# Optimization experiments

Measured on AMD Instinct MI355X. Metric: run time of the kernel, lower is better.

The kernel has to match this reference:

```python
import jax, jax.numpy as jnp
import numpy as np

NEG_INF = -1.0e9  # matches the -1000000000.0 additive mask in the source


def setup_inputs() -> dict:
    key = jax.random.key(0)
    kq, kk, kv = jax.random.split(key, 3)
    B, Lq, Lk, D = 16, 2048, 2048, 128
    q = jax.random.normal(kq, (B, Lq, D), dtype=jnp.float32)
    k = jax.random.normal(kk, (B, Lk, D), dtype=jnp.float32)
    v = jax.random.normal(kv, (B, Lk, D), dtype=jnp.float32)
    mask = jnp.ones((B, Lq, Lk), dtype=jnp.int32)  # 1 = attend, 0 = blocked
    return {"q": q, "k": k, "v": v, "mask": mask}


def reference(q, k, v, mask):
    # temper = sqrt(d_k)
    temper = jnp.sqrt(jnp.asarray(q.shape[-1], dtype=jnp.float32))
    # scores: [B, Lq, Lk] = batch_dot(q, k, axes=[2,2]) / temper
    scores = jnp.einsum("bqd,bkd->bqk", q, k) / temper
    # additive mask: -1e9 * (1 - mask)
    scores = scores + NEG_INF * (1.0 - mask.astype(jnp.float32))
    attn = jax.nn.softmax(scores, axis=-1)
    # dropout is identity at inference time
    out = jnp.einsum("bqk,bkd->bqd", attn, v)
    return (out, attn)
```

## Files before the change

kernel.cpp:

```cpp
#include <hip/hip_runtime.h>

typedef __bf16 bf16_t;
typedef __bf16 bf16x8 __attribute__((ext_vector_type(8)));
typedef __bf16 bf16x4 __attribute__((ext_vector_type(4)));
typedef float  f32x4  __attribute__((ext_vector_type(4)));
typedef int    i32x4  __attribute__((ext_vector_type(4)));

#define B_      16
#define L_      2048
#define D_      128
#define QTB     128
#define NEGINF  (-1.0e9f)
#define SCALE   0.08838834764831845f

#define MFMA_BF16 __builtin_amdgcn_mfma_f32_16x16x32_bf16

#define BARRIER() do { asm volatile("s_waitcnt lgkmcnt(0)" ::: "memory"); \
                       __builtin_amdgcn_s_barrier(); } while (0)

__global__ __launch_bounds__(256) void prep_kernel(
    const float* __restrict__ k, const float* __restrict__ v,
    bf16_t* __restrict__ kb, bf16_t* __restrict__ vt)
{
    __shared__ bf16_t tile[128 * 144];
    const int tid = threadIdx.x;
    const int bid = (int)blockIdx.x;

    if (bid < 256) {
        const int b  = bid >> 4;
        const int l0 = (bid & 15) * 128;
        #pragma unroll
        for (int it = 0; it < 16; ++it) {
            int idx = tid + it * 256;
            int row = idx >> 5;
            int dc4 = idx & 31;
            f32x4 x = __builtin_nontemporal_load(
                (const f32x4*)(v + ((size_t)b * L_ + l0 + row) * (size_t)D_ + dc4 * 4));
            #pragma unroll
            for (int i = 0; i < 4; ++i) tile[(dc4 * 4 + i) * 144 + row] = (bf16_t)x[i];
        }
        __syncthreads();
        #pragma unroll
        for (int it = 0; it < 8; ++it) {
            int idx = tid + it * 256;
            int d   = idx >> 4;
            int lc  = idx & 15;
            bf16x8 vec = *(const bf16x8*)&tile[d * 144 + lc * 8];
            *(bf16x8*)(vt + ((size_t)b * D_ + d) * (size_t)L_ + l0 + lc * 8) = vec;
        }
    } else {
        const int idx0 = (bid - 256) * 256 + tid;
        #pragma unroll
        for (int c = 0; c < 16; ++c) {
            int idx = idx0 + c * 65536;
            f32x4 x = __builtin_nontemporal_load((const f32x4*)(k + (size_t)idx * 4));
            bf16x4 o;
            #pragma unroll
            for (int i = 0; i < 4; ++i) o[i] = (bf16_t)x[i];
            *(bf16x4*)(kb + (size_t)idx * 4) = o;
        }
    }
}

template <bool WS>
__global__ __launch_bounds__(512, 1) void sdpa_kernel(
    const float* __restrict__ q, const float* __restrict__ k,
    const float* __restrict__ v, const int* __restrict__ mask,
    const bf16_t* __restrict__ kb, const bf16_t* __restrict__ vt,
    float* __restrict__ out, float* __restrict__ attn)
{
    __shared__ char     KstRaw[3 * 8192];
    __shared__ char     MVRaw[3 * 16384];
    __shared__ unsigned mlds[8 * 1024];
    __shared__ bf16_t   plds[8][16][40];

    const int tid = threadIdx.x;
    const int w   = tid >> 6;
    const int l   = tid & 63;
    const int li  = l & 15;
    const int lg  = l >> 4;

    const int bid  = (int)blockIdx.x;
    const int bid2 = (bid & 7) * 32 + (bid >> 3);
    const int b    = bid2 >> 4;
    const int qt   = bid2 & 15;
    const int qbase = qt * QTB;

    const size_t bq   = (size_t)b * L_;
    const int    qrow = qbase + w * 16 + li;

    const float*  qp   = q  + (bq + qbase) * (size_t)D_;
    const bf16_t* kbp  = kb + bq * (size_t)D_;
    const float*  kp   = k  + bq * (size_t)D_;
    const bf16_t* vtp  = vt + (size_t)b * D_ * (size_t)L_;
    const float*  vp   = v  + bq * (size_t)D_;
    float* attnrow = attn + (bq + qrow) * (size_t)L_;
    float* outp    = out  + (bq + qbase) * (size_t)D_;

    bf16x8 aq[4];
    #pragma unroll
    for (int ds = 0; ds < 4; ++ds) {
        const float* p = qp + (size_t)(w * 16 + li) * D_ + ds * 32 + lg * 8;
        f32x4 x0 = *(const f32x4*)p;
        f32x4 x1 = *(const f32x4*)(p + 4);
        bf16x8 a;
        #pragma unroll
        for (int u = 0; u < 4; ++u) {
            a[u]     = (bf16_t)(x0[u] * SCALE);
            a[4 + u] = (bf16_t)(x1[u] * SCALE);
        }
        aq[ds] = a;
    }

    const int krow = tid >> 4, kslot = tid & 15;
    const int kdst = krow * 256 + ((kslot * 16) ^ ((krow & 7) << 4));
    const int mrow = tid >> 3, mslot = tid & 7;
    const int mdst0 = mrow * 128 + ((mslot * 16) ^ ((mrow & 7) << 4));
    const int mdst1 = (mrow + 64) * 128 + ((mslot * 16) ^ ((mrow & 7) << 4));
    const int vrow = tid >> 2, vslot = tid & 3;
    const int vdst = vrow * 64 + vslot * 16;

    const bf16_t* ksrcb = kbp + (size_t)krow * D_ + kslot * 8;
    const float*  ksrcf = kp  + (size_t)krow * D_ + kslot * 8;
    const int*    msrc0 = mask + (size_t)(bq + qbase + mrow) * L_ + mslot * 4;
    const int*    msrc1 = mask + (size_t)(bq + qbase + mrow + 64) * L_ + mslot * 4;
    const bf16_t* vsrcb = vtp + (size_t)vrow * L_ + vslot * 8;

    auto issueK = [&](int c, i32x4& ri, f32x4& rf0, f32x4& rf1) {
        if constexpr (WS) {
            ri = *(const i32x4*)(ksrcb + (size_t)c * 32 * D_);
        } else {
            rf0 = *(const f32x4*)(ksrcf + (size_t)c * 32 * D_);
            rf1 = *(const f32x4*)(ksrcf + (size_t)c * 32 * D_ + 4);
        }
    };
    auto writeK = [&](int sl, const i32x4& ri, const f32x4& rf0, const f32x4& rf1) {
        char* d = KstRaw + sl * 8192 + kdst;
        if constexpr (WS) {
            *(i32x4*)d = ri;
        } else {
            bf16x8 o;
            #pragma unroll
            for (int u = 0; u < 4; ++u) { o[u] = (bf16_t)rf0[u]; o[4+u] = (bf16_t)rf1[u]; }
            *(bf16x8*)d = o;
        }
    };
    auto issueM = [&](int c, i32x4& m0, i32x4& m1) {
        m0 = __builtin_nontemporal_load((const i32x4*)(msrc0 + c * 32));
        m1 = __builtin_nontemporal_load((const i32x4*)(msrc1 + c * 32));
    };
    auto writeM = [&](int sl, const i32x4& m0, const i32x4& m1) {
        *(i32x4*)(MVRaw + sl * 16384 + mdst0) = m0;
        *(i32x4*)(MVRaw + sl * 16384 + mdst1) = m1;
    };
    auto issueV = [&](int c, i32x4& ri, float (&vf)[8]) {
        if constexpr (WS) {
            ri = *(const i32x4*)(vsrcb + c * 32);
        } else {
            #pragma unroll
            for (int u = 0; u < 8; ++u)
                vf[u] = vp[(size_t)(c * 32 + vslot * 8 + u) * D_ + vrow];
        }
    };
    auto writeV = [&](int sl, const i32x4& ri, const float (&vf)[8]) {
        char* d = MVRaw + sl * 16384 + vdst;
        if constexpr (WS) {
            *(i32x4*)d = ri;
        } else {
            bf16x8 o;
            #pragma unroll
            for (int u = 0; u < 8; ++u) o[u] = (bf16_t)vf[u];
            *(bf16x8*)d = o;
        }
    };

    const int xr = (li & 7) << 4;

    auto qkt = [&](int sl, f32x4& a0, f32x4& a1) {
        const char* Ks = KstRaw + sl * 8192;
        f32x4 r0 = {0.f,0.f,0.f,0.f}, r1 = {0.f,0.f,0.f,0.f};
        #pragma unroll
        for (int ds = 0; ds < 4; ++ds) {
            bf16x8 k0 = *(const bf16x8*)(Ks + li * 256 + ((ds * 64 + lg * 16) ^ xr));
            r0 = MFMA_BF16(k0, aq[ds], r0, 0, 0, 0);
        }
        #pragma unroll
        for (int ds = 0; ds < 4; ++ds) {
            bf16x8 k1 = *(const bf16x8*)(Ks + (16 + li) * 256 + ((ds * 64 + lg * 16) ^ xr));
            r1 = MFMA_BF16(k1, aq[ds], r1, 0, 0, 0);
        }
        a0 = r0; a1 = r1;
    };

    float m_run = -3.4e38f, l_run = 0.f;
    {
        unsigned mword = 0;
        auto p1c = [&](int c, int sl) {
            f32x4 a0, a1;
            qkt(sl, a0, a1);
            const char* Ms = MVRaw + sl * 16384 + (w * 16 + li) * 128;
            i32x4 va  = *(const i32x4*)(Ms + ((lg * 16) ^ xr));
            i32x4 vb_ = *(const i32x4*)(Ms + ((64 + lg * 16) ^ xr));
            unsigned byte =
                (va[0]  != 0 ?   1u : 0u) | (va[1]  != 0 ?   2u : 0u) |
                (va[2]  != 0 ?   4u : 0u) | (va[3]  != 0 ?   8u : 0u) |
                (vb_[0] != 0 ?  16u : 0u) | (vb_[1] != 0 ?  32u : 0u) |
                (vb_[2] != 0 ?  64u : 0u) | (vb_[3] != 0 ? 128u : 0u);
            float s0[4], s1[4];
            #pragma unroll
            for (int r = 0; r < 4; ++r) {
                s0[r] = a0[r] + (((byte >> r)       & 1u) ? 0.f : NEGINF);
                s1[r] = a1[r] + (((byte >> (4 + r)) & 1u) ? 0.f : NEGINF);
            }
            float mx = fmaxf(fmaxf(fmaxf(s0[0], s0[1]), fmaxf(s0[2], s0[3])),
                             fmaxf(fmaxf(s1[0], s1[1]), fmaxf(s1[2], s1[3])));
            mx = fmaxf(mx, m_run);
            float acc = 0.f;
            #pragma unroll
            for (int r = 0; r < 4; ++r)
                acc += __expf(s0[r] - mx) + __expf(s1[r] - mx);
            l_run = l_run * __expf(m_run - mx) + acc;
            m_run = mx;
            mword |= byte << ((c & 3) * 8);
            if ((c & 3) == 3) { mlds[w * 1024 + (c >> 2) * 64 + l] = mword; mword = 0; }
        };

        i32x4 kA{}, kB{}, mA0{}, mA1{}, mB0{}, mB1{};
        f32x4 kfA0{}, kfA1{}, kfB0{}, kfB1{};
        issueK(0, kA, kfA0, kfA1); issueM(0, mA0, mA1);
        issueK(1, kB, kfB0, kfB1); issueM(1, mB0, mB1);
        writeK(0, kA, kfA0, kfA1); writeM(0, mA0, mA1);
        BARRIER();
        int s0i = 0, s1i = 1, s2i = 2;
        #pragma unroll 1
        for (int c = 0; c < 64; c += 2) {
            if (c + 2 < 64) { issueK(c + 2, kA, kfA0, kfA1); issueM(c + 2, mA0, mA1); }
            writeK(s1i, kB, kfB0, kfB1); writeM(s1i, mB0, mB1);
            BARRIER();
            p1c(c, s0i);
            { int t = s0i; s0i = s1i; s1i = s2i; s2i = t; }
            if (c + 3 < 64) { issueK(c + 3, kB, kfB0, kfB1); issueM(c + 3, mB0, mB1); }
            if (c + 2 < 64) { writeK(s1i, kA, kfA0, kfA1); writeM(s1i, mA0, mA1); }
            BARRIER();
            p1c(c + 1, s0i);
            { int t = s0i; s0i = s1i; s1i = s2i; s2i = t; }
        }
    }

    #pragma unroll
    for (int off = 16; off < 64; off <<= 1) {
        float mo = __shfl_xor(m_run, off);
        float lo = __shfl_xor(l_run, off);
        float mn = fmaxf(m_run, mo);
        l_run = l_run * __expf(m_run - mn) + lo * __expf(mo - mn);
        m_run = mn;
    }
    const float inv_l = 1.f / l_run;

    f32x4 pv[8];
    #pragma unroll
    for (int dt = 0; dt < 8; ++dt) pv[dt] = {0.f, 0.f, 0.f, 0.f};

    {
        auto p2c = [&](int c, int sl) {
            f32x4 a0, a1;
            qkt(sl, a0, a1);
            const unsigned mw = mlds[w * 1024 + (c >> 2) * 64 + l];
            const unsigned byte = (mw >> ((c & 3) * 8)) & 0xffu;
            f32x4 o0, o1; bf16x4 pb0, pb1;
            #pragma unroll
            for (int r = 0; r < 4; ++r) {
                float sa = a0[r] + (((byte >> r)       & 1u) ? 0.f : NEGINF);
                float sb = a1[r] + (((byte >> (4 + r)) & 1u) ? 0.f : NEGINF);
                float p0 = __expf(sa - m_run);
                float p1 = __expf(sb - m_run);
                o0[r] = p0 * inv_l;  o1[r] = p1 * inv_l;
                pb0[r] = (bf16_t)p0; pb1[r] = (bf16_t)p1;
            }
            __builtin_nontemporal_store(o0, (f32x4*)(attnrow + c * 32 + lg * 4));
            __builtin_nontemporal_store(o1, (f32x4*)(attnrow + c * 32 + 16 + lg * 4));
            *(bf16x4*)&plds[w][li][lg * 4]      = pb0;
            *(bf16x4*)&plds[w][li][16 + lg * 4] = pb1;
            bf16x8 pa = *(const bf16x8*)&plds[w][li][lg * 8];
            const char* Vs = MVRaw + sl * 16384;
            #pragma unroll
            for (int dt = 0; dt < 8; ++dt) {
                bf16x8 vbf = *(const bf16x8*)(Vs + (dt * 16 + li) * 64 + lg * 16);
                pv[dt] = MFMA_BF16(pa, vbf, pv[dt], 0, 0, 0);
            }
        };

        BARRIER();
        i32x4 kA{}, kB{}, vA{}, vB{};
        f32x4 kfA0{}, kfA1{}, kfB0{}, kfB1{};
        float vfA[8], vfB[8];
        issueK(0, kA, kfA0, kfA1); issueV(0, vA, vfA);
        issueK(1, kB, kfB0, kfB1); issueV(1, vB, vfB);
        writeK(0, kA, kfA0, kfA1); writeV(0, vA, vfA);
        BARRIER();
        int s0i = 0, s1i = 1, s2i = 2;
        #pragma unroll 1
        for (int c = 0; c < 64; c += 2) {
            if (c + 2 < 64) { issueK(c + 2, kA, kfA0, kfA1); issueV(c + 2, vA, vfA); }
            writeK(s1i, kB, kfB0, kfB1); writeV(s1i, vB, vfB);
            BARRIER();
            p2c(c, s0i);
            { int t = s0i; s0i = s1i; s1i = s2i; s2i = t; }
            if (c + 3 < 64) { issueK(c + 3, kB, kfB0, kfB1); issueV(c + 3, vB, vfB); }
            if (c + 2 < 64) { writeK(s1i, kA, kfA0, kfA1); writeV(s1i, vA, vfA); }
            BARRIER();
            p2c(c + 1, s0i);
            { int t = s0i; s0i = s1i; s1i = s2i; s2i = t; }
        }
    }

    #pragma unroll
    for (int r = 0; r < 4; ++r) {
        const float il = __shfl(inv_l, lg * 4 + r);
        float* orow = outp + (size_t)(w * 16 + lg * 4 + r) * D_ + li;
        #pragma unroll
        for (int dt = 0; dt < 8; ++dt)
            __builtin_nontemporal_store(pv[dt][r] * il, orow + dt * 16);
    }
}

extern "C" void kernel_launch(void* const* d_in, const int* in_sizes, int n_in,
                              void* d_out, int out_size, void* d_ws, size_t ws_size,
                              hipStream_t stream) {
    const float* q    = (const float*)d_in[0];
    const float* k    = (const float*)d_in[1];
    const float* v    = (const float*)d_in[2];
    const int*   mask = (const int*)d_in[3];

    float* out  = (float*)d_out;
    float* attn = out + (size_t)B_ * L_ * D_;

    const size_t VT_BYTES = (size_t)B_ * D_ * L_ * 2;
    const size_t KB_BYTES = (size_t)B_ * L_ * D_ * 2;
    const bool ws_ok = ws_size >= VT_BYTES + KB_BYTES;
    bf16_t* vt = (bf16_t*)d_ws;
    bf16_t* kb = (bf16_t*)((char*)d_ws + VT_BYTES);

    if (ws_ok) {
        hipLaunchKernelGGL(prep_kernel, dim3(512), dim3(256), 0, stream, k, v, kb, vt);
        hipLaunchKernelGGL(sdpa_kernel<true>, dim3(256), dim3(512), 0, stream,
                           q, k, v, mask, kb, vt, out, attn);
    } else {
        hipLaunchKernelGGL(sdpa_kernel<false>, dim3(256), dim3(512), 0, stream,
                           q, k, v, mask, kb, vt, out, attn);
    }
}
```

Baseline: 183.2 us.

## Halve query tile to 64 rows, launch 512 blocks of 256 threads

```diff
diff --git a/kernel.cpp b/kernel.cpp
--- a/kernel.cpp
+++ b/kernel.cpp
@@ -9,7 +9,7 @@
 #define B_      16
 #define L_      2048
 #define D_      128
-#define QTB     128
+#define QTB     64
 #define NEGINF  (-1.0e9f)
 #define SCALE   0.08838834764831845f
 
@@ -63,16 +63,16 @@
 }
 
 template <bool WS>
-__global__ __launch_bounds__(512, 1) void sdpa_kernel(
+__global__ __launch_bounds__(256, 1) void sdpa_kernel(
     const float* __restrict__ q, const float* __restrict__ k,
     const float* __restrict__ v, const int* __restrict__ mask,
     const bf16_t* __restrict__ kb, const bf16_t* __restrict__ vt,
     float* __restrict__ out, float* __restrict__ attn)
 {
-    __shared__ char     KstRaw[3 * 8192];
-    __shared__ char     MVRaw[3 * 16384];
-    __shared__ unsigned mlds[8 * 1024];
-    __shared__ bf16_t   plds[8][16][40];
+    __shared__ char     Kst[3][8192];
+    __shared__ char     Vst[3][8192];
+    __shared__ unsigned mbits[64 * 64];
+    __shared__ bf16_t   plds[4][16][40];
 
     const int tid = threadIdx.x;
     const int w   = tid >> 6;
@@ -81,20 +81,19 @@
     const int lg  = l >> 4;
 
     const int bid  = (int)blockIdx.x;
-    const int bid2 = (bid & 7) * 32 + (bid >> 3);
-    const int b    = bid2 >> 4;
-    const int qt   = bid2 & 15;
+    const int bid2 = (bid & 7) * 64 + (bid >> 3);
+    const int b    = bid2 >> 5;
+    const int qt   = bid2 & 31;
     const int qbase = qt * QTB;
 
-    const size_t bq   = (size_t)b * L_;
-    const int    qrow = qbase + w * 16 + li;
+    const size_t bq = (size_t)b * L_;
 
     const float*  qp   = q  + (bq + qbase) * (size_t)D_;
     const bf16_t* kbp  = kb + bq * (size_t)D_;
     const float*  kp   = k  + bq * (size_t)D_;
     const bf16_t* vtp  = vt + (size_t)b * D_ * (size_t)L_;
     const float*  vp   = v  + bq * (size_t)D_;
-    float* attnrow = attn + (bq + qrow) * (size_t)L_;
+    float* attnrow = attn + (bq + qbase + (size_t)(w * 16 + li)) * (size_t)L_;
     float* outp    = out  + (bq + qbase) * (size_t)D_;
 
     bf16x8 aq[4];
@@ -112,72 +111,87 @@
         aq[ds] = a;
     }
 
-    const int krow = tid >> 4, kslot = tid & 15;
-    const int kdst = krow * 256 + ((kslot * 16) ^ ((krow & 7) << 4));
-    const int mrow = tid >> 3, mslot = tid & 7;
-    const int mdst0 = mrow * 128 + ((mslot * 16) ^ ((mrow & 7) << 4));
-    const int mdst1 = (mrow + 64) * 128 + ((mslot * 16) ^ ((mrow & 7) << 4));
-    const int vrow = tid >> 2, vslot = tid & 3;
-    const int vdst = vrow * 64 + vslot * 16;
-
-    const bf16_t* ksrcb = kbp + (size_t)krow * D_ + kslot * 8;
-    const float*  ksrcf = kp  + (size_t)krow * D_ + kslot * 8;
-    const int*    msrc0 = mask + (size_t)(bq + qbase + mrow) * L_ + mslot * 4;
-    const int*    msrc1 = mask + (size_t)(bq + qbase + mrow + 64) * L_ + mslot * 4;
-    const bf16_t* vsrcb = vtp + (size_t)vrow * L_ + vslot * 8;
-
-    auto issueK = [&](int c, i32x4& ri, f32x4& rf0, f32x4& rf1) {
+    const int krow = tid >> 3, ks = tid & 7;
+    const int kdst = krow * 256 + ((ks * 16) ^ ((krow & 7) << 4));
+    const bf16_t* ksrcb = kbp + (size_t)krow * D_ + ks * 8;
+    const float*  ksrcf = kp  + (size_t)krow * D_ + ks * 8;
+
+    const int vrow = tid >> 1, vs = tid & 1;
+    const int vswz = (vrow >> 1) & 3;
+    const int vdst0 = vrow * 64 + (((vs * 2)     ^ vswz) << 4);
+    const int vdst1 = vrow * 64 + (((vs * 2 + 1) ^ vswz) << 4);
+    const bf16_t* vsrcb = vtp + (size_t)vrow * L_;
+
+    const int mr = tid & 63;
+    const int* msrc = mask + (size_t)(bq + qbase + mr) * L_ + w * 8;
+
+    auto issueK = [&](int c, i32x4& r0, i32x4& r1, f32x4* rf) {
         if constexpr (WS) {
-            ri = *(const i32x4*)(ksrcb + (size_t)c * 32 * D_);
+            r0 = *(const i32x4*)(ksrcb + (size_t)c * 32 * D_);
+            r1 = *(const i32x4*)(ksrcb + (size_t)c * 32 * D_ + 64);
         } else {
-            rf0 = *(const f32x4*)(ksrcf + (size_t)c * 32 * D_);
-            rf1 = *(const f32x4*)(ksrcf + (size_t)c * 32 * D_ + 4);
-        }
-    };
-    auto writeK = [&](int sl, const i32x4& ri, const f32x4& rf0, const f32x4& rf1) {
-        char* d = KstRaw + sl * 8192 + kdst;
+            rf[0] = *(const f32x4*)(ksrcf + (size_t)c * 32 * D_);
+            rf[1] = *(const f32x4*)(ksrcf + (size_t)c * 32 * D_ + 4);
+            rf[2] = *(const f32x4*)(ksrcf + (size_t)c * 32 * D_ + 64);
+            rf[3] = *(const f32x4*)(ksrcf + (size_t)c * 32 * D_ + 68);
+        }
+    };
+    auto writeK = [&](int sl, const i32x4& r0, const i32x4& r1, const f32x4* rf) {
+        char* d = Kst[sl] + kdst;
         if constexpr (WS) {
-            *(i32x4*)d = ri;
+            *(i32x4*)d = r0;
+            *(i32x4*)(d + 128) = r1;
         } else {
-            bf16x8 o;
-            #pragma unroll
-            for (int u = 0; u < 4; ++u) { o[u] = (bf16_t)rf0[u]; o[4+u] = (bf16_t)rf1[u]; }
-            *(bf16x8*)d = o;
+            bf16x8 o0, o1;
+            #pragma unroll
+            for (int u = 0; u < 4; ++u) {
+                o0[u] = (bf16_t)rf[0][u]; o0[4+u] = (bf16_t)rf[1][u];
+                o1[u] = (bf16_t)rf[2][u]; o1[4+u] = (bf16_t)rf[3][u];
+            }
+            *(bf16x8*)d = o0;
+            *(bf16x8*)(d + 128) = o1;
         }
     };
     auto issueM = [&](int c, i32x4& m0, i32x4& m1) {
-        m0 = __builtin_nontemporal_load((const i32x4*)(msrc0 + c * 32));
-        m1 = __builtin_nontemporal_load((const i32x4*)(msrc1 + c * 32));
-    };
-    auto writeM = [&](int sl, const i32x4& m0, const i32x4& m1) {
-        *(i32x4*)(MVRaw + sl * 16384 + mdst0) = m0;
-        *(i32x4*)(MVRaw + sl * 16384 + mdst1) = m1;
-    };
-    auto issueV = [&](int c, i32x4& ri, float (&vf)[8]) {
+        m0 = __builtin_nontemporal_load((const i32x4*)(msrc + c * 32));
+        m1 = __builtin_nontemporal_load((const i32x4*)(msrc + c * 32 + 4));
+    };
+    auto writeM = [&](int c, const i32x4& m0, const i32x4& m1) {
+        unsigned by = (m0[0] != 0 ?   1u : 0u) | (m0[1] != 0 ?   2u : 0u)
+                    | (m0[2] != 0 ?   4u : 0u) | (m0[3] != 0 ?   8u : 0u)
+                    | (m1[0] != 0 ?  16u : 0u) | (m1[1] != 0 ?  32u : 0u)
+                    | (m1[2] != 0 ?  64u : 0u) | (m1[3] != 0 ? 128u : 0u);
+        ((char*)mbits)[c * 256 + mr * 4 + w] = (char)by;
+    };
+    auto issueV = [&](int c, i32x4& r0, i32x4& r1, float* vf) {
         if constexpr (WS) {
-            ri = *(const i32x4*)(vsrcb + c * 32);
+            r0 = *(const i32x4*)(vsrcb + c * 32 + vs * 16);
+            r1 = *(const i32x4*)(vsrcb + c * 32 + vs * 16 + 8);
         } else {
             #pragma unroll
-            for (int u = 0; u < 8; ++u)
-                vf[u] = vp[(size_t)(c * 32 + vslot * 8 + u) * D_ + vrow];
-        }
-    };
-    auto writeV = [&](int sl, const i32x4& ri, const float (&vf)[8]) {
-        char* d = MVRaw + sl * 16384 + vdst;
+            for (int u = 0; u < 8; ++u) {
+                vf[u]     = vp[(size_t)(c * 32 + vs * 16 + u) * D_ + vrow];
+                vf[8 + u] = vp[(size_t)(c * 32 + vs * 16 + 8 + u) * D_ + vrow];
+            }
+        }
+    };
+    auto writeV = [&](int sl, const i32x4& r0, const i32x4& r1, const float* vf) {
         if constexpr (WS) {
-            *(i32x4*)d = ri;
+            *(i32x4*)(Vst[sl] + vdst0) = r0;
+            *(i32x4*)(Vst[sl] + vdst1) = r1;
         } else {
-            bf16x8 o;
-            #pragma unroll
-            for (int u = 0; u < 8; ++u) o[u] = (bf16_t)vf[u];
-            *(bf16x8*)d = o;
+            bf16x8 o0, o1;
+            #pragma unroll
+            for (int u = 0; u < 8; ++u) { o0[u] = (bf16_t)vf[u]; o1[u] = (bf16_t)vf[8+u]; }
+            *(bf16x8*)(Vst[sl] + vdst0) = o0;
+            *(bf16x8*)(Vst[sl] + vdst1) = o1;
         }
     };
 
     const int xr = (li & 7) << 4;
 
     auto qkt = [&](int sl, f32x4& a0, f32x4& a1) {
-        const char* Ks = KstRaw + sl * 8192;
+        const char* Ks = Kst[sl];
         f32x4 r0 = {0.f,0.f,0.f,0.f}, r1 = {0.f,0.f,0.f,0.f};
         #pragma unroll
         for (int ds = 0; ds < 4; ++ds) {
@@ -191,21 +205,17 @@
         }
         a0 = r0; a1 = r1;
     };
+    auto maskbyte = [&](int c) -> unsigned {
+        unsigned word = mbits[c * 64 + w * 16 + li];
+        return ((word >> (lg * 4)) & 0xFu) | (((word >> (16 + lg * 4)) & 0xFu) << 4);
+    };
 
     float m_run = -3.4e38f, l_run = 0.f;
     {
-        unsigned mword = 0;
         auto p1c = [&](int c, int sl) {
             f32x4 a0, a1;
             qkt(sl, a0, a1);
-            const char* Ms = MVRaw + sl * 16384 + (w * 16 + li) * 128;
-            i32x4 va  = *(const i32x4*)(Ms + ((lg * 16) ^ xr));
-            i32x4 vb_ = *(const i32x4*)(Ms + ((64 + lg * 16) ^ xr));
-            unsigned byte =
-                (va[0]  != 0 ?   1u : 0u) | (va[1]  != 0 ?   2u : 0u) |
-                (va[2]  != 0 ?   4u : 0u) | (va[3]  != 0 ?   8u : 0u) |
-                (vb_[0] != 0 ?  16u : 0u) | (vb_[1] != 0 ?  32u : 0u) |
-                (vb_[2] != 0 ?  64u : 0u) | (vb_[3] != 0 ? 128u : 0u);
+            const unsigned byte = maskbyte(c);
             float s0[4], s1[4];
             #pragma unroll
             for (int r = 0; r < 4; ++r) {
@@ -221,26 +231,24 @@
                 acc += __expf(s0[r] - mx) + __expf(s1[r] - mx);
             l_run = l_run * __expf(m_run - mx) + acc;
             m_run = mx;
-            mword |= byte << ((c & 3) * 8);
-            if ((c & 3) == 3) { mlds[w * 1024 + (c >> 2) * 64 + l] = mword; mword = 0; }
         };
 
-        i32x4 kA{}, kB{}, mA0{}, mA1{}, mB0{}, mB1{};
-        f32x4 kfA0{}, kfA1{}, kfB0{}, kfB1{};
-        issueK(0, kA, kfA0, kfA1); issueM(0, mA0, mA1);
-        issueK(1, kB, kfB0, kfB1); issueM(1, mB0, mB1);
-        writeK(0, kA, kfA0, kfA1); writeM(0, mA0, mA1);
+        i32x4 kA0{}, kA1{}, kB0{}, kB1{}, mA0{}, mA1{}, mB0{}, mB1{};
+        f32x4 kfA[4], kfB[4];
+        issueK(0, kA0, kA1, kfA); issueM(0, mA0, mA1);
+        issueK(1, kB0, kB1, kfB); issueM(1, mB0, mB1);
+        writeK(0, kA0, kA1, kfA); writeM(0, mA0, mA1);
         BARRIER();
         int s0i = 0, s1i = 1, s2i = 2;
         #pragma unroll 1
         for (int c = 0; c < 64; c += 2) {
-            if (c + 2 < 64) { issueK(c + 2, kA, kfA0, kfA1); issueM(c + 2, mA0, mA1); }
-            writeK(s1i, kB, kfB0, kfB1); writeM(s1i, mB0, mB1);
+            if (c + 2 < 64) { issueK(c + 2, kA0, kA1, kfA); issueM(c + 2, mA0, mA1); }
+            writeK(s1i, kB0, kB1, kfB); writeM(c + 1, mB0, mB1);
             BARRIER();
             p1c(c, s0i);
             { int t = s0i; s0i = s1i; s1i = s2i; s2i = t; }
-            if (c + 3 < 64) { issueK(c + 3, kB, kfB0, kfB1); issueM(c + 3, mB0, mB1); }
-            if (c + 2 < 64) { writeK(s1i, kA, kfA0, kfA1); writeM(s1i, mA0, mA1); }
+            if (c + 3 < 64) { issueK(c + 3, kB0, kB1, kfB); issueM(c + 3, mB0, mB1); }
+            if (c + 2 < 64) { writeK(s1i, kA0, kA1, kfA); writeM(c + 2, mA0, mA1); }
             BARRIER();
             p1c(c + 1, s0i);
             { int t = s0i; s0i = s1i; s1i = s2i; s2i = t; }
@@ -265,8 +273,7 @@
         auto p2c = [&](int c, int sl) {
             f32x4 a0, a1;
             qkt(sl, a0, a1);
-            const unsigned mw = mlds[w * 1024 + (c >> 2) * 64 + l];
-            const unsigned byte = (mw >> ((c & 3) * 8)) & 0xffu;
+            const unsigned byte = maskbyte(c);
             f32x4 o0, o1; bf16x4 pb0, pb1;
             #pragma unroll
             for (int r = 0; r < 4; ++r) {
@@ -282,32 +289,33 @@
             *(bf16x4*)&plds[w][li][lg * 4]      = pb0;
             *(bf16x4*)&plds[w][li][16 + lg * 4] = pb1;
             bf16x8 pa = *(const bf16x8*)&plds[w][li][lg * 8];
-            const char* Vs = MVRaw + sl * 16384;
+            const char* Vs = Vst[sl];
             #pragma unroll
             for (int dt = 0; dt < 8; ++dt) {
-                bf16x8 vbf = *(const bf16x8*)(Vs + (dt * 16 + li) * 64 + lg * 16);
+                const int vr = dt * 16 + li;
+                bf16x8 vbf = *(const bf16x8*)(Vs + vr * 64 + (((lg ^ ((li >> 1) & 3))) << 4));
                 pv[dt] = MFMA_BF16(pa, vbf, pv[dt], 0, 0, 0);
             }
         };
 
         BARRIER();
-        i32x4 kA{}, kB{}, vA{}, vB{};
-        f32x4 kfA0{}, kfA1{}, kfB0{}, kfB1{};
-        float vfA[8], vfB[8];
-        issueK(0, kA, kfA0, kfA1); issueV(0, vA, vfA);
-        issueK(1, kB, kfB0, kfB1); issueV(1, vB, vfB);
-        writeK(0, kA, kfA0, kfA1); writeV(0, vA, vfA);
+        i32x4 kA0{}, kA1{}, kB0{}, kB1{}, vA0{}, vA1{}, vB0{}, vB1{};
+        f32x4 kfA[4], kfB[4];
+        float vfA[16], vfB[16];
+        issueK(0, kA0, kA1, kfA); issueV(0, vA0, vA1, vfA);
+        issueK(1, kB0, kB1, kfB); issueV(1, vB0, vB1, vfB);
+        writeK(0, kA0, kA1, kfA); writeV(0, vA0, vA1, vfA);
         BARRIER();
         int s0i = 0, s1i = 1, s2i = 2;
         #pragma unroll 1
         for (int c = 0; c < 64; c += 2) {
-            if (c + 2 < 64) { issueK(c + 2, kA, kfA0, kfA1); issueV(c + 2, vA, vfA); }
-            writeK(s1i, kB, kfB0, kfB1); writeV(s1i, vB, vfB);
+            if (c + 2 < 64) { issueK(c + 2, kA0, kA1, kfA); issueV(c + 2, vA0, vA1, vfA); }
+            writeK(s1i, kB0, kB1, kfB); writeV(s1i, vB0, vB1, vfB);
             BARRIER();
             p2c(c, s0i);
             { int t = s0i; s0i = s1i; s1i = s2i; s2i = t; }
-            if (c + 3 < 64) { issueK(c + 3, kB, kfB0, kfB1); issueV(c + 3, vB, vfB); }
-            if (c + 2 < 64) { writeK(s1i, kA, kfA0, kfA1); writeV(s1i, vA, vfA); }
+            if (c + 3 < 64) { issueK(c + 3, kB0, kB1, kfB); issueV(c + 3, vB0, vB1, vfB); }
+            if (c + 2 < 64) { writeK(s1i, kA0, kA1, kfA); writeV(s1i, vA0, vA1, vfA); }
             BARRIER();
             p2c(c + 1, s0i);
             { int t = s0i; s0i = s1i; s1i = s2i; s2i = t; }
@@ -343,10 +351,10 @@
 
     if (ws_ok) {
         hipLaunchKernelGGL(prep_kernel, dim3(512), dim3(256), 0, stream, k, v, kb, vt);
-        hipLaunchKernelGGL(sdpa_kernel<true>, dim3(256), dim3(512), 0, stream,
+        hipLaunchKernelGGL(sdpa_kernel<true>, dim3(512), dim3(256), 0, stream,
                            q, k, v, mask, kb, vt, out, attn);
     } else {
-        hipLaunchKernelGGL(sdpa_kernel<false>, dim3(256), dim3(512), 0, stream,
+        hipLaunchKernelGGL(sdpa_kernel<false>, dim3(512), dim3(256), 0, stream,
                            q, k, v, mask, kb, vt, out, attn);
     }
 }
```

New measurement: 276.0 us. +50.6%, slower.

## Store K/V tiles in MFMA-fragment order and pack mask into bit bytes at load

Applied to the files above, without the earlier changes.

```diff
diff --git a/kernel.cpp b/kernel.cpp
--- a/kernel.cpp
+++ b/kernel.cpp
@@ -69,9 +69,9 @@
     const bf16_t* __restrict__ kb, const bf16_t* __restrict__ vt,
     float* __restrict__ out, float* __restrict__ attn)
 {
-    __shared__ char     KstRaw[3 * 8192];
-    __shared__ char     MVRaw[3 * 16384];
-    __shared__ unsigned mlds[8 * 1024];
+    __shared__ char     Kst[3][8192];
+    __shared__ char     Vst[3][8192];
+    __shared__ unsigned mbits[64 * 128];
     __shared__ bf16_t   plds[8][16][40];
 
     const int tid = threadIdx.x;
@@ -86,15 +86,14 @@
     const int qt   = bid2 & 15;
     const int qbase = qt * QTB;
 
-    const size_t bq   = (size_t)b * L_;
-    const int    qrow = qbase + w * 16 + li;
-
-    const float*  qp   = q  + (bq + qbase) * (size_t)D_;
-    const bf16_t* kbp  = kb + bq * (size_t)D_;
-    const float*  kp   = k  + bq * (size_t)D_;
-    const bf16_t* vtp  = vt + (size_t)b * D_ * (size_t)L_;
-    const float*  vp   = v  + bq * (size_t)D_;
-    float* attnrow = attn + (bq + qrow) * (size_t)L_;
+    const size_t bq = (size_t)b * L_;
+
+    const float*  qp  = q  + (bq + qbase) * (size_t)D_;
+    const bf16_t* kbp = kb + bq * (size_t)D_;
+    const float*  kp  = k  + bq * (size_t)D_;
+    const bf16_t* vtp = vt + (size_t)b * D_ * (size_t)L_;
+    const float*  vp  = v  + bq * (size_t)D_;
+    float* attnrow = attn + (bq + qbase + (size_t)(w * 16 + li)) * (size_t)L_;
     float* outp    = out  + (bq + qbase) * (size_t)D_;
 
     bf16x8 aq[4];
@@ -112,19 +111,14 @@
         aq[ds] = a;
     }
 
-    const int krow = tid >> 4, kslot = tid & 15;
-    const int kdst = krow * 256 + ((kslot * 16) ^ ((krow & 7) << 4));
-    const int mrow = tid >> 3, mslot = tid & 7;
-    const int mdst0 = mrow * 128 + ((mslot * 16) ^ ((mrow & 7) << 4));
-    const int mdst1 = (mrow + 64) * 128 + ((mslot * 16) ^ ((mrow & 7) << 4));
-    const int vrow = tid >> 2, vslot = tid & 3;
-    const int vdst = vrow * 64 + vslot * 16;
-
-    const bf16_t* ksrcb = kbp + (size_t)krow * D_ + kslot * 8;
-    const float*  ksrcf = kp  + (size_t)krow * D_ + kslot * 8;
-    const int*    msrc0 = mask + (size_t)(bq + qbase + mrow) * L_ + mslot * 4;
-    const int*    msrc1 = mask + (size_t)(bq + qbase + mrow + 64) * L_ + mslot * 4;
-    const bf16_t* vsrcb = vtp + (size_t)vrow * L_ + vslot * 8;
+    const int ku_t  = (tid >> 6) & 1, ku_ds = tid >> 7;
+    const int ku_lg = (tid >> 4) & 3, ku_li = tid & 15;
+    const bf16_t* ksrcb = kbp + (size_t)(ku_t * 16 + ku_li) * D_ + ku_ds * 32 + ku_lg * 8;
+    const float*  ksrcf = kp  + (size_t)(ku_t * 16 + ku_li) * D_ + ku_ds * 32 + ku_lg * 8;
+    const int vu_d = (tid >> 6) * 16 + (tid & 15);
+    const int vu_lg = (tid >> 4) & 3;
+    const bf16_t* vsrcb = vtp + (size_t)vu_d * L_ + vu_lg * 8;
+    const int uofs = tid * 16;
 
     auto issueK = [&](int c, i32x4& ri, f32x4& rf0, f32x4& rf1) {
         if constexpr (WS) {
@@ -135,7 +129,7 @@
         }
     };
     auto writeK = [&](int sl, const i32x4& ri, const f32x4& rf0, const f32x4& rf1) {
-        char* d = KstRaw + sl * 8192 + kdst;
+        char* d = Kst[sl] + uofs;
         if constexpr (WS) {
             *(i32x4*)d = ri;
         } else {
@@ -145,25 +139,17 @@
             *(bf16x8*)d = o;
         }
     };
-    auto issueM = [&](int c, i32x4& m0, i32x4& m1) {
-        m0 = __builtin_nontemporal_load((const i32x4*)(msrc0 + c * 32));
-        m1 = __builtin_nontemporal_load((const i32x4*)(msrc1 + c * 32));
-    };
-    auto writeM = [&](int sl, const i32x4& m0, const i32x4& m1) {
-        *(i32x4*)(MVRaw + sl * 16384 + mdst0) = m0;
-        *(i32x4*)(MVRaw + sl * 16384 + mdst1) = m1;
-    };
     auto issueV = [&](int c, i32x4& ri, float (&vf)[8]) {
         if constexpr (WS) {
             ri = *(const i32x4*)(vsrcb + c * 32);
         } else {
             #pragma unroll
             for (int u = 0; u < 8; ++u)
-                vf[u] = vp[(size_t)(c * 32 + vslot * 8 + u) * D_ + vrow];
+                vf[u] = vp[(size_t)(c * 32 + vu_lg * 8 + u) * D_ + vu_d];
         }
     };
     auto writeV = [&](int sl, const i32x4& ri, const float (&vf)[8]) {
-        char* d = MVRaw + sl * 16384 + vdst;
+        char* d = Vst[sl] + uofs;
         if constexpr (WS) {
             *(i32x4*)d = ri;
         } else {
@@ -174,19 +160,36 @@
         }
     };
 
-    const int xr = (li & 7) << 4;
+    const int mr = tid & 127, wg = tid >> 7;
+    const int* msrc = mask + (size_t)(bq + qbase + mr) * L_ + wg * 8;
+    auto issueM = [&](int c, i32x4& m0, i32x4& m1) {
+        m0 = __builtin_nontemporal_load((const i32x4*)(msrc + c * 32));
+        m1 = __builtin_nontemporal_load((const i32x4*)(msrc + c * 32 + 4));
+    };
+    auto writeM = [&](int c, const i32x4& m0, const i32x4& m1) {
+        unsigned by = (m0[0] != 0 ?   1u : 0u) | (m0[1] != 0 ?   2u : 0u)
+                    | (m0[2] != 0 ?   4u : 0u) | (m0[3] != 0 ?   8u : 0u)
+                    | (m1[0] != 0 ?  16u : 0u) | (m1[1] != 0 ?  32u : 0u)
+                    | (m1[2] != 0 ?  64u : 0u) | (m1[3] != 0 ? 128u : 0u);
+        ((char*)mbits)[c * 512 + mr * 4 + wg] = (char)by;
+    };
+    auto maskbyte = [&](int c) -> unsigned {
+        unsigned word = mbits[c * 128 + w * 16 + li];
+        return ((word >> (lg * 4)) & 0xFu) | (((word >> (16 + lg * 4)) & 0xFu) << 4);
+    };
 
     auto qkt = [&](int sl, f32x4& a0, f32x4& a1) {
-        const char* Ks = KstRaw + sl * 8192;
+        const char* Ks = Kst[sl];
+        const int bo = lg * 256 + li * 16;
         f32x4 r0 = {0.f,0.f,0.f,0.f}, r1 = {0.f,0.f,0.f,0.f};
         #pragma unroll
         for (int ds = 0; ds < 4; ++ds) {
-            bf16x8 k0 = *(const bf16x8*)(Ks + li * 256 + ((ds * 64 + lg * 16) ^ xr));
+            bf16x8 k0 = *(const bf16x8*)(Ks + (ds * 2 + 0) * 1024 + bo);
             r0 = MFMA_BF16(k0, aq[ds], r0, 0, 0, 0);
         }
         #pragma unroll
         for (int ds = 0; ds < 4; ++ds) {
-            bf16x8 k1 = *(const bf16x8*)(Ks + (16 + li) * 256 + ((ds * 64 + lg * 16) ^ xr));
+            bf16x8 k1 = *(const bf16x8*)(Ks + (ds * 2 + 1) * 1024 + bo);
             r1 = MFMA_BF16(k1, aq[ds], r1, 0, 0, 0);
         }
         a0 = r0; a1 = r1;
@@ -194,18 +197,10 @@
 
     float m_run = -3.4e38f, l_run = 0.f;
     {
-        unsigned mword = 0;
         auto p1c = [&](int c, int sl) {
             f32x4 a0, a1;
             qkt(sl, a0, a1);
-            const char* Ms = MVRaw + sl * 16384 + (w * 16 + li) * 128;
-            i32x4 va  = *(const i32x4*)(Ms + ((lg * 16) ^ xr));
-            i32x4 vb_ = *(const i32x4*)(Ms + ((64 + lg * 16) ^ xr));
-            unsigned byte =
-                (va[0]  != 0 ?   1u : 0u) | (va[1]  != 0 ?   2u : 0u) |
-                (va[2]  != 0 ?   4u : 0u) | (va[3]  != 0 ?   8u : 0u) |
-                (vb_[0] != 0 ?  16u : 0u) | (vb_[1] != 0 ?  32u : 0u) |
-                (vb_[2] != 0 ?  64u : 0u) | (vb_[3] != 0 ? 128u : 0u);
+            const unsigned byte = maskbyte(c);
             float s0[4], s1[4];
             #pragma unroll
             for (int r = 0; r < 4; ++r) {
@@ -221,8 +216,6 @@
                 acc += __expf(s0[r] - mx) + __expf(s1[r] - mx);
             l_run = l_run * __expf(m_run - mx) + acc;
             m_run = mx;
-            mword |= byte << ((c & 3) * 8);
-            if ((c & 3) == 3) { mlds[w * 1024 + (c >> 2) * 64 + l] = mword; mword = 0; }
         };
 
         i32x4 kA{}, kB{}, mA0{}, mA1{}, mB0{}, mB1{};
@@ -235,12 +228,12 @@
         #pragma unroll 1
         for (int c = 0; c < 64; c += 2) {
             if (c + 2 < 64) { issueK(c + 2, kA, kfA0, kfA1); issueM(c + 2, mA0, mA1); }
-            writeK(s1i, kB, kfB0, kfB1); writeM(s1i, mB0, mB1);
+            writeK(s1i, kB, kfB0, kfB1); writeM(c + 1, mB0, mB1);
             BARRIER();
             p1c(c, s0i);
             { int t = s0i; s0i = s1i; s1i = s2i; s2i = t; }
             if (c + 3 < 64) { issueK(c + 3, kB, kfB0, kfB1); issueM(c + 3, mB0, mB1); }
-            if (c + 2 < 64) { writeK(s1i, kA, kfA0, kfA1); writeM(s1i, mA0, mA1); }
+            if (c + 2 < 64) { writeK(s1i, kA, kfA0, kfA1); writeM(c + 2, mA0, mA1); }
             BARRIER();
             p1c(c + 1, s0i);
             { int t = s0i; s0i = s1i; s1i = s2i; s2i = t; }
@@ -265,8 +258,7 @@
         auto p2c = [&](int c, int sl) {
             f32x4 a0, a1;
             qkt(sl, a0, a1);
-            const unsigned mw = mlds[w * 1024 + (c >> 2) * 64 + l];
-            const unsigned byte = (mw >> ((c & 3) * 8)) & 0xffu;
+            const unsigned byte = maskbyte(c);
             f32x4 o0, o1; bf16x4 pb0, pb1;
             #pragma unroll
             for (int r = 0; r < 4; ++r) {
@@ -282,10 +274,11 @@
             *(bf16x4*)&plds[w][li][lg * 4]      = pb0;
             *(bf16x4*)&plds[w][li][16 + lg * 4] = pb1;
             bf16x8 pa = *(const bf16x8*)&plds[w][li][lg * 8];
-            const char* Vs = MVRaw + sl * 16384;
+            const char* Vs = Vst[sl];
+            const int bo = lg * 256 + li * 16;
             #pragma unroll
             for (int dt = 0; dt < 8; ++dt) {
-                bf16x8 vbf = *(const bf16x8*)(Vs + (dt * 16 + li) * 64 + lg * 16);
+                bf16x8 vbf = *(const bf16x8*)(Vs + dt * 1024 + bo);
                 pv[dt] = MFMA_BF16(pa, vbf, pv[dt], 0, 0, 0);
             }
         };
```

After: 310.1 us. 1.69x slower.

## Switch to double-buffered 64-key tiles with one barrier per tile

Applied to the files above, without the earlier changes.

```diff
diff --git a/kernel.cpp b/kernel.cpp
--- a/kernel.cpp
+++ b/kernel.cpp
@@ -69,8 +69,8 @@
     const bf16_t* __restrict__ kb, const bf16_t* __restrict__ vt,
     float* __restrict__ out, float* __restrict__ attn)
 {
-    __shared__ char     KstRaw[3 * 8192];
-    __shared__ char     MVRaw[3 * 16384];
+    __shared__ char     Kst[2][16384];
+    __shared__ char     MV[2][32768];
     __shared__ unsigned mlds[8 * 1024];
     __shared__ bf16_t   plds[8][16][40];
 
@@ -86,15 +86,14 @@
     const int qt   = bid2 & 15;
     const int qbase = qt * QTB;
 
-    const size_t bq   = (size_t)b * L_;
-    const int    qrow = qbase + w * 16 + li;
-
-    const float*  qp   = q  + (bq + qbase) * (size_t)D_;
-    const bf16_t* kbp  = kb + bq * (size_t)D_;
-    const float*  kp   = k  + bq * (size_t)D_;
-    const bf16_t* vtp  = vt + (size_t)b * D_ * (size_t)L_;
-    const float*  vp   = v  + bq * (size_t)D_;
-    float* attnrow = attn + (bq + qrow) * (size_t)L_;
+    const size_t bq = (size_t)b * L_;
+
+    const float*  qp  = q  + (bq + qbase) * (size_t)D_;
+    const bf16_t* kbp = kb + bq * (size_t)D_;
+    const float*  kp  = k  + bq * (size_t)D_;
+    const bf16_t* vtp = vt + (size_t)b * D_ * (size_t)L_;
+    const float*  vp  = v  + bq * (size_t)D_;
+    float* attnrow = attn + (bq + qbase + (size_t)(w * 16 + li)) * (size_t)L_;
     float* outp    = out  + (bq + qbase) * (size_t)D_;
 
     bf16x8 aq[4];
@@ -114,70 +113,88 @@
 
     const int krow = tid >> 4, kslot = tid & 15;
     const int kdst = krow * 256 + ((kslot * 16) ^ ((krow & 7) << 4));
+    const bf16_t* ksrcb = kbp + (size_t)krow * D_ + kslot * 8;
+    const float*  ksrcf = kp  + (size_t)krow * D_ + kslot * 8;
+
     const int mrow = tid >> 3, mslot = tid & 7;
     const int mdst0 = mrow * 128 + ((mslot * 16) ^ ((mrow & 7) << 4));
     const int mdst1 = (mrow + 64) * 128 + ((mslot * 16) ^ ((mrow & 7) << 4));
+    const int*    msrc0 = mask + (size_t)(bq + qbase + mrow) * L_ + mslot * 4;
+    const int*    msrc1 = mask + (size_t)(bq + qbase + mrow + 64) * L_ + mslot * 4;
+
     const int vrow = tid >> 2, vslot = tid & 3;
     const int vdst = vrow * 64 + vslot * 16;
-
-    const bf16_t* ksrcb = kbp + (size_t)krow * D_ + kslot * 8;
-    const float*  ksrcf = kp  + (size_t)krow * D_ + kslot * 8;
-    const int*    msrc0 = mask + (size_t)(bq + qbase + mrow) * L_ + mslot * 4;
-    const int*    msrc1 = mask + (size_t)(bq + qbase + mrow + 64) * L_ + mslot * 4;
     const bf16_t* vsrcb = vtp + (size_t)vrow * L_ + vslot * 8;
 
-    auto issueK = [&](int c, i32x4& ri, f32x4& rf0, f32x4& rf1) {
-        if constexpr (WS) {
-            ri = *(const i32x4*)(ksrcb + (size_t)c * 32 * D_);
-        } else {
-            rf0 = *(const f32x4*)(ksrcf + (size_t)c * 32 * D_);
-            rf1 = *(const f32x4*)(ksrcf + (size_t)c * 32 * D_ + 4);
-        }
-    };
-    auto writeK = [&](int sl, const i32x4& ri, const f32x4& rf0, const f32x4& rf1) {
-        char* d = KstRaw + sl * 8192 + kdst;
-        if constexpr (WS) {
-            *(i32x4*)d = ri;
-        } else {
-            bf16x8 o;
-            #pragma unroll
-            for (int u = 0; u < 4; ++u) { o[u] = (bf16_t)rf0[u]; o[4+u] = (bf16_t)rf1[u]; }
-            *(bf16x8*)d = o;
-        }
-    };
-    auto issueM = [&](int c, i32x4& m0, i32x4& m1) {
-        m0 = __builtin_nontemporal_load((const i32x4*)(msrc0 + c * 32));
-        m1 = __builtin_nontemporal_load((const i32x4*)(msrc1 + c * 32));
-    };
-    auto writeM = [&](int sl, const i32x4& m0, const i32x4& m1) {
-        *(i32x4*)(MVRaw + sl * 16384 + mdst0) = m0;
-        *(i32x4*)(MVRaw + sl * 16384 + mdst1) = m1;
-    };
-    auto issueV = [&](int c, i32x4& ri, float (&vf)[8]) {
-        if constexpr (WS) {
-            ri = *(const i32x4*)(vsrcb + c * 32);
-        } else {
-            #pragma unroll
-            for (int u = 0; u < 8; ++u)
-                vf[u] = vp[(size_t)(c * 32 + vslot * 8 + u) * D_ + vrow];
-        }
-    };
-    auto writeV = [&](int sl, const i32x4& ri, const float (&vf)[8]) {
-        char* d = MVRaw + sl * 16384 + vdst;
-        if constexpr (WS) {
-            *(i32x4*)d = ri;
-        } else {
-            bf16x8 o;
-            #pragma unroll
-            for (int u = 0; u < 8; ++u) o[u] = (bf16_t)vf[u];
-            *(bf16x8*)d = o;
+    auto issueK = [&](int t, i32x4 (&ri)[2], f32x4 (&rf)[2][2]) {
+        #pragma unroll
+        for (int s = 0; s < 2; ++s) {
+            if constexpr (WS) {
+                ri[s] = *(const i32x4*)(ksrcb + (size_t)(t * 64 + s * 32) * D_);
+            } else {
+                rf[s][0] = *(const f32x4*)(ksrcf + (size_t)(t * 64 + s * 32) * D_);
+                rf[s][1] = *(const f32x4*)(ksrcf + (size_t)(t * 64 + s * 32) * D_ + 4);
+            }
+        }
+    };
+    auto writeK = [&](int sl, const i32x4 (&ri)[2], const f32x4 (&rf)[2][2]) {
+        #pragma unroll
+        for (int s = 0; s < 2; ++s) {
+            char* d = Kst[sl] + s * 8192 + kdst;
+            if constexpr (WS) {
+                *(i32x4*)d = ri[s];
+            } else {
+                bf16x8 o;
+                #pragma unroll
+                for (int u = 0; u < 4; ++u) { o[u] = (bf16_t)rf[s][0][u]; o[4+u] = (bf16_t)rf[s][1][u]; }
+                *(bf16x8*)d = o;
+            }
+        }
+    };
+    auto issueM = [&](int t, i32x4 (&m0)[2], i32x4 (&m1)[2]) {
+        #pragma unroll
+        for (int s = 0; s < 2; ++s) {
+            m0[s] = __builtin_nontemporal_load((const i32x4*)(msrc0 + t * 64 + s * 32));
+            m1[s] = __builtin_nontemporal_load((const i32x4*)(msrc1 + t * 64 + s * 32));
+        }
+    };
+    auto writeM = [&](int sl, const i32x4 (&m0)[2], const i32x4 (&m1)[2]) {
+        #pragma unroll
+        for (int s = 0; s < 2; ++s) {
+            *(i32x4*)(MV[sl] + s * 16384 + mdst0) = m0[s];
+            *(i32x4*)(MV[sl] + s * 16384 + mdst1) = m1[s];
+        }
+    };
+    auto issueV = [&](int t, i32x4 (&ri)[2], float (&vf)[2][8]) {
+        #pragma unroll
+        for (int s = 0; s < 2; ++s) {
+            if constexpr (WS) {
+                ri[s] = *(const i32x4*)(vsrcb + t * 64 + s * 32);
+            } else {
+                #pragma unroll
+                for (int u = 0; u < 8; ++u)
+                    vf[s][u] = vp[(size_t)(t * 64 + s * 32 + vslot * 8 + u) * D_ + vrow];
+            }
+        }
+    };
+    auto writeV = [&](int sl, const i32x4 (&ri)[2], const float (&vf)[2][8]) {
+        #pragma unroll
+        for (int s = 0; s < 2; ++s) {
+            char* d = MV[sl] + s * 8192 + vdst;
+            if constexpr (WS) {
+                *(i32x4*)d = ri[s];
+            } else {
+                bf16x8 o;
+                #pragma unroll
+                for (int u = 0; u < 8; ++u) o[u] = (bf16_t)vf[s][u];
+                *(bf16x8*)d = o;
+            }
         }
     };
 
     const int xr = (li & 7) << 4;
 
-    auto qkt = [&](int sl, f32x4& a0, f32x4& a1) {
-        const char* Ks = KstRaw + sl * 8192;
+    auto qkt = [&](const char* Ks, f32x4& a0, f32x4& a1) {
         f32x4 r0 = {0.f,0.f,0.f,0.f}, r1 = {0.f,0.f,0.f,0.f};
         #pragma unroll
         for (int ds = 0; ds < 4; ++ds) {
@@ -195,10 +212,10 @@
     float m_run = -3.4e38f, l_run = 0.f;
     {
         unsigned mword = 0;
-        auto p1c = [&](int c, int sl) {
+        auto p1c = [&](int m, int sl, int s) {
             f32x4 a0, a1;
-            qkt(sl, a0, a1);
-            const char* Ms = MVRaw + sl * 16384 + (w * 16 + li) * 128;
+            qkt(Kst[sl] + s * 8192, a0, a1);
+            const char* Ms = MV[sl] + s * 16384 + (w * 16 + li) * 128;
             i32x4 va  = *(const i32x4*)(Ms + ((lg * 16) ^ xr));
             i32x4 vb_ = *(const i32x4*)(Ms + ((64 + lg * 16) ^ xr));
             unsigned byte =
@@ -221,29 +238,23 @@
                 acc += __expf(s0[r] - mx) + __expf(s1[r] - mx);
             l_run = l_run * __expf(m_run - mx) + acc;
             m_run = mx;
-            mword |= byte << ((c & 3) * 8);
-            if ((c & 3) == 3) { mlds[w * 1024 + (c >> 2) * 64 + l] = mword; mword = 0; }
+            mword |= byte << ((m & 3) * 8);
+            if ((m & 3) == 3) { mlds[w * 1024 + (m >> 2) * 64 + l] = mword; mword = 0; }
         };
 
-        i32x4 kA{}, kB{}, mA0{}, mA1{}, mB0{}, mB1{};
-        f32x4 kfA0{}, kfA1{}, kfB0{}, kfB1{};
-        issueK(0, kA, kfA0, kfA1); issueM(0, mA0, mA1);
-        issueK(1, kB, kfB0, kfB1); issueM(1, mB0, mB1);
-        writeK(0, kA, kfA0, kfA1); writeM(0, mA0, mA1);
+        i32x4 kr[2]{}, m0r[2]{}, m1r[2]{};
+        f32x4 kf[2][2];
+        issueK(0, kr, kf); issueM(0, m0r, m1r);
+        writeK(0, kr, kf); writeM(0, m0r, m1r);
         BARRIER();
-        int s0i = 0, s1i = 1, s2i = 2;
         #pragma unroll 1
-        for (int c = 0; c < 64; c += 2) {
-            if (c + 2 < 64) { issueK(c + 2, kA, kfA0, kfA1); issueM(c + 2, mA0, mA1); }
-            writeK(s1i, kB, kfB0, kfB1); writeM(s1i, mB0, mB1);
+        for (int t = 0; t < 32; ++t) {
+            const int sl = t & 1;
+            if (t + 1 < 32) { issueK(t + 1, kr, kf); issueM(t + 1, m0r, m1r); }
+            p1c(2 * t,     sl, 0);
+            p1c(2 * t + 1, sl, 1);
+            if (t + 1 < 32) { writeK(sl ^ 1, kr, kf); writeM(sl ^ 1, m0r, m1r); }
             BARRIER();
-            p1c(c, s0i);
-            { int t = s0i; s0i = s1i; s1i = s2i; s2i = t; }
-            if (c + 3 < 64) { issueK(c + 3, kB, kfB0, kfB1); issueM(c + 3, mB0, mB1); }
-            if (c + 2 < 64) { writeK(s1i, kA, kfA0, kfA1); writeM(s1i, mA0, mA1); }
-            BARRIER();
-            p1c(c + 1, s0i);
-            { int t = s0i; s0i = s1i; s1i = s2i; s2i = t; }
         }
     }
 
@@ -262,11 +273,11 @@
     for (int dt = 0; dt < 8; ++dt) pv[dt] = {0.f, 0.f, 0.f, 0.f};
 
     {
-        auto p2c = [&](int c, int sl) {
+        auto p2c = [&](int m, int sl, int s) {
             f32x4 a0, a1;
-            qkt(sl, a0, a1);
-            const unsigned mw = mlds[w * 1024 + (c >> 2) * 64 + l];
-            const unsigned byte = (mw >> ((c & 3) * 8)) & 0xffu;
+            qkt(Kst[sl] + s * 8192, a0, a1);
+            const unsigned mw = mlds[w * 1024 + (m >> 2) * 64 + l];
+            const unsigned byte = (mw >> ((m & 3) * 8)) & 0xffu;
             f32x4 o0, o1; bf16x4 pb0, pb1;
             #pragma unroll
             for (int r = 0; r < 4; ++r) {
@@ -277,12 +288,12 @@
                 o0[r] = p0 * inv_l;  o1[r] = p1 * inv_l;
                 pb0[r] = (bf16_t)p0; pb1[r] = (bf16_t)p1;
             }
-            __builtin_nontemporal_store(o0, (f32x4*)(attnrow + c * 32 + lg * 4));
-            __builtin_nontemporal_store(o1, (f32x4*)(attnrow + c * 32 + 16 + lg * 4));
+            __builtin_nontemporal_store(o0, (f32x4*)(attnrow + m * 32 + lg * 4));
+            __builtin_nontemporal_store(o1, (f32x4*)(attnrow + m * 32 + 16 + lg * 4));
             *(bf16x4*)&plds[w][li][lg * 4]      = pb0;
             *(bf16x4*)&plds[w][li][16 + lg * 4] = pb1;
             bf16x8 pa = *(const bf16x8*)&plds[w][li][lg * 8];
-            const char* Vs = MVRaw + sl * 16384;
+            const char* Vs = MV[sl] + s * 8192;
             #pragma unroll
             for (int dt = 0; dt < 8; ++dt) {
                 bf16x8 vbf = *(const bf16x8*)(Vs + (dt * 16 + li) * 64 + lg * 16);
@@ -290,27 +301,20 @@
             }
         };
 
+        i32x4 kr[2]{}, vr[2]{};
+        f32x4 kf[2][2];
+        float vf[2][8];
+        issueK(0, kr, kf); issueV(0, vr, vf);
+        writeK(0, kr, kf); writeV(0, vr, vf);
         BARRIER();
-        i32x4 kA{}, kB{}, vA{}, vB{};
-        f32x4 kfA0{}, kfA1{}, kfB0{}, kfB1{};
-        float vfA[8], vfB[8];
-        issueK(0, kA, kfA0, kfA1); issueV(0, vA, vfA);
-        issueK(1, kB, kfB0, kfB1); issueV(1, vB, vfB);
-        writeK(0, kA, kfA0, kfA1); writeV(0, vA, vfA);
-        BARRIER();
-        int s0i = 0, s1i = 1, s2i = 2;
         #pragma unroll 1
-        for (int c = 0; c < 64; c += 2) {
-            if (c + 2 < 64) { issueK(c + 2, kA, kfA0, kfA1); issueV(c + 2, vA, vfA); }
-            writeK(s1i, kB, kfB0, kfB1); writeV(s1i, vB, vfB);
+        for (int t = 0; t < 32; ++t) {
+            const int sl = t & 1;
+            if (t + 1 < 32) { issueK(t + 1, kr, kf); issueV(t + 1, vr, vf); }
+            p2c(2 * t,     sl, 0);
+            p2c(2 * t + 1, sl, 1);
+            if (t + 1 < 32) { writeK(sl ^ 1, kr, kf); writeV(sl ^ 1, vr, vf); }
             BARRIER();
-            p2c(c, s0i);
-            { int t = s0i; s0i = s1i; s1i = s2i; s2i = t; }
-            if (c + 3 < 64) { issueK(c + 3, kB, kfB0, kfB1); issueV(c + 3, vB, vfB); }
-            if (c + 2 < 64) { writeK(s1i, kA, kfA0, kfA1); writeV(s1i, vA, vfA); }
-            BARRIER();
-            p2c(c + 1, s0i);
-            { int t = s0i; s0i = s1i; s1i = s2i; s2i = t; }
         }
     }
 
```

Result: no change. 183.9 us (+0.4%).
